# Optimization experiments

Hardware: AMD Instinct MI355X
Metric: run time of the kernel (lower is better)

The kernel has to match this reference:

```python
import jax, jax.numpy as jnp
import numpy as np

H = 32        # num_attention_heads
DN = 128      # qk_nope_head_dim
DR = 64       # qk_rope_head_dim
DV = 128      # v_head_dim
DQ = DN + DR  # q_head_dim
HID = 4096
NEG_INF = -1e30


def setup_inputs() -> dict:
    key = jax.random.key(0)
    k0, k1, k2, k3 = jax.random.split(key, 4)
    B, S = 4, 1024
    hidden_states = jax.random.normal(k0, (B, S, HID), dtype=jnp.float32)
    wq = jax.random.normal(k1, (HID, H * DQ), dtype=jnp.float32) * 0.02
    wkv = jax.random.normal(k2, (HID, H * (DN + DV) + DR), dtype=jnp.float32) * 0.02
    wo = jax.random.normal(k3, (H * DV, HID), dtype=jnp.float32) * 0.02
    return {"hidden_states": hidden_states, "wq": wq, "wkv": wkv, "wo": wo}


def reference(hidden_states, wq, wkv, wo):
    B, S, D = hidden_states.shape
    # q_proj -> [B, S, H, DQ]; attention only uses the nope part q[..., :DN]
    q = jnp.einsum('bsd,de->bse', hidden_states, wq).reshape(B, S, H, DQ)
    kv = jnp.einsum('bsd,de->bse', hidden_states, wkv)
    k = kv[..., : H * DN].reshape(B, S, H, DN)
    v = kv[..., H * DN : H * (DN + DV)].reshape(B, S, H, DV)
    # rope columns kv[..., H*(DN+DV):] are computed by kv_proj but unused, as in source
    scale = DQ ** -0.5  # note: scale uses full q_head_dim (192), per source
    scores = jnp.einsum('bqhd,bkhd->bhqk', q[..., :DN], k) * scale
    causal = jnp.tril(jnp.ones((S, S), dtype=bool))  # [q, k]
    scores = jnp.where(causal[None, None], scores, NEG_INF)
    probs = jax.nn.softmax(scores, axis=-1)
    attn = jnp.einsum('bhqk,bkhd->bqhd', probs, v).reshape(B, S, H * DV)
    return jnp.einsum('bse,ed->bsd', attn, wo)
```

## Files before the change

kernel.cpp:

```cpp
#include <hip/hip_runtime.h>


typedef __attribute__((ext_vector_type(4))) float f32x4;
typedef _Float16 half8 __attribute__((ext_vector_type(8)));
typedef _Float16 half4 __attribute__((ext_vector_type(4)));

#define AS3(p) ((__attribute__((address_space(3))) void*)(p))
#define AS1(p) ((__attribute__((address_space(1))) void*)(void*)(p))

__global__ __launch_bounds__(256) void k_convert(const float* __restrict__ src,
                                                 _Float16* __restrict__ dst) {
  int i = (blockIdx.x * 256 + threadIdx.x) * 8;
  float4 a = *(const float4*)(src + i);
  float4 b = *(const float4*)(src + i + 4);
  half8 v = { (_Float16)a.x, (_Float16)a.y, (_Float16)a.z, (_Float16)a.w,
              (_Float16)b.x, (_Float16)b.y, (_Float16)b.z, (_Float16)b.w };
  *(half8*)(dst + i) = v;
}

__global__ __launch_bounds__(256) void k_tc_qkv(const float* __restrict__ wq,
                                                const float* __restrict__ wkv,
                                                _Float16* __restrict__ out) {
  __shared__ __align__(16) _Float16 t[64][72];
  int k0 = blockIdx.x * 64;
  int c0 = blockIdx.y * 64;
  int tid = threadIdx.x;
  int rl = tid >> 4;
  int cl4 = (tid & 15) << 2;
  int c = c0 + cl4;
#pragma unroll
  for (int i = 0; i < 4; ++i) {
    int r = k0 + rl + i * 16;
    const float* sp;
    if (c0 < 4096) sp = wq + (size_t)r * 6144 + ((c >> 7) * 192 + (c & 127));
    else           sp = wkv + (size_t)r * 8256 + (c - 4096);
    float4 v = *(const float4*)sp;
    t[cl4 + 0][rl + i * 16] = (_Float16)v.x;
    t[cl4 + 1][rl + i * 16] = (_Float16)v.y;
    t[cl4 + 2][rl + i * 16] = (_Float16)v.z;
    t[cl4 + 3][rl + i * 16] = (_Float16)v.w;
  }
  __syncthreads();
  int r4 = (tid & 15) << 2;
#pragma unroll
  for (int i = 0; i < 4; ++i) {
    int cl = (tid >> 4) + i * 16;
    half4 p = { t[cl][r4], t[cl][r4 + 1], t[cl][r4 + 2], t[cl][r4 + 3] };
    *(half4*)(out + (size_t)(c0 + cl) * 4096 + k0 + r4) = p;
  }
}

__global__ __launch_bounds__(256) void k_tc_wo(const float* __restrict__ wo,
                                               _Float16* __restrict__ out) {
  __shared__ __align__(16) _Float16 t[64][72];
  int k0 = blockIdx.x * 64;
  int c0 = blockIdx.y * 64;
  int tid = threadIdx.x;
  int rl = tid >> 4;
  int cl4 = (tid & 15) << 2;
#pragma unroll
  for (int i = 0; i < 4; ++i) {
    int r = k0 + rl + i * 16;
    float4 v = *(const float4*)(wo + (size_t)r * 4096 + c0 + cl4);
    t[cl4 + 0][rl + i * 16] = (_Float16)v.x;
    t[cl4 + 1][rl + i * 16] = (_Float16)v.y;
    t[cl4 + 2][rl + i * 16] = (_Float16)v.z;
    t[cl4 + 3][rl + i * 16] = (_Float16)v.w;
  }
  __syncthreads();
  int r4 = (tid & 15) << 2;
#pragma unroll
  for (int i = 0; i < 4; ++i) {
    int cl = (tid >> 4) + i * 16;
    half4 p = { t[cl][r4], t[cl][r4 + 1], t[cl][r4 + 2], t[cl][r4 + 3] };
    *(half4*)(out + (size_t)(c0 + cl) * 4096 + k0 + r4) = p;
  }
}


#define A_OFF(d, h) ((d) * 32768 + (h) * 16384)
#define B_OFF(d, h) (65536 + (d) * 32768 + (h) * 16384)

#define STAGE(gbase, ldsoff, ktb)                                              \
  do {                                                                         \
    _Pragma("unroll") for (int i_ = 0; i_ < 2; ++i_) {                         \
      int c_ = w * 2 + i_;                                                     \
      int row_ = c_ * 16 + (lane >> 2);                                        \
      int ss_ = (lane & 3) ^ ((lane >> 3) & 3);                                \
      __builtin_amdgcn_global_load_lds(                                        \
          AS1((gbase) + (size_t)row_ * ldb + (ktb) + ss_ * 16),                \
          AS3(lds + (ldsoff) + c_ * 1024), 16, 0, 0);                          \
    }                                                                          \
  } while (0)

#define LDA(dst, d, ks, fm)                                                    \
  do {                                                                         \
    int r_ = wr * 128 + (fm) * 16 + (lane & 15);                               \
    int sl_ = (lane >> 4) ^ ((r_ >> 1) & 3);                                   \
    dst = *(const half8*)(lds + (d) * 32768 + (ks) * 16384 + r_ * 64 +         \
                          sl_ * 16);                                           \
  } while (0)

#define LDB(dst, d, ks, fn)                                                    \
  do {                                                                         \
    int r_ = wc * 64 + (fn) * 16 + (lane & 15);                                \
    int sl_ = (lane >> 4) ^ ((r_ >> 1) & 3);                                   \
    dst = *(const half8*)(lds + 65536 + (d) * 32768 + (ks) * 16384 +           \
                          r_ * 64 + sl_ * 16);                                 \
  } while (0)

#define BARRIER()                                                              \
  do {                                                                         \
    asm volatile("" ::: "memory");                                             \
    __builtin_amdgcn_s_barrier();                                              \
    asm volatile("" ::: "memory");                                             \
  } while (0)

#define MFMA16(mh)                                                             \
  do {                                                                         \
    __builtin_amdgcn_s_setprio(1);                                             \
    _Pragma("unroll") for (int mi_ = 0; mi_ < 4; ++mi_)                        \
        _Pragma("unroll") for (int ni_ = 0; ni_ < 4; ++ni_)                    \
            acc[(mh) * 4 + mi_][ni_] = __builtin_amdgcn_mfma_f32_16x16x32_f16( \
                af[mi_], bfr[ni_], acc[(mh) * 4 + mi_][ni_], 0, 0, 0);         \
    __builtin_amdgcn_s_setprio(0);                                             \
  } while (0)

__global__ __launch_bounds__(512, 2) void k_gemm256(
    const _Float16* __restrict__ A, const _Float16* __restrict__ Bt,
    void* __restrict__ outp, int M, int N, int K, int mode, int ntn, int nblk) {
  extern __shared__ __align__(16) char lds[];
  int tid = threadIdx.x, lane = tid & 63, w = tid >> 6;
  int wr = w >> 2, wc = w & 3;
  int bid = blockIdx.x;
  int sid = (bid & 7) * (nblk >> 3) + (bid >> 3);
  int mt = sid / ntn, nt = sid % ntn;
  int m0 = mt * 256, n0 = nt * 256;

  const char* Ab = (const char*)(A + (size_t)m0 * K);
  const char* Bb = (const char*)(Bt + (size_t)n0 * K);
  size_t ldb = (size_t)K * 2;

  f32x4 acc[8][4];
#pragma unroll
  for (int i = 0; i < 8; ++i)
#pragma unroll
    for (int j = 0; j < 4; ++j) acc[i][j] = (f32x4){0.f, 0.f, 0.f, 0.f};
  half8 af[4], bfr[4];

  int NT = K >> 6;
  STAGE(Ab, A_OFF(0, 0), 0);
  STAGE(Bb, B_OFF(0, 0), 0);
  STAGE(Ab, A_OFF(0, 1), 64);
  STAGE(Bb, B_OFF(0, 1), 64);
  STAGE(Ab, A_OFF(1, 0), 128);
  STAGE(Bb, B_OFF(1, 0), 128);
  asm volatile("s_waitcnt vmcnt(4)" ::: "memory");
  BARRIER();

  for (int k = 0; k < NT; ++k) {
    int d = k & 1, dn = d ^ 1;
    int ktb1 = (k + 1) << 7, ktb2 = (k + 2) << 7;
    bool s1 = (k + 1 < NT), s2 = (k + 2 < NT);
    LDB(bfr[0], d, 0, 0); LDB(bfr[1], d, 0, 1);
    LDB(bfr[2], d, 0, 2); LDB(bfr[3], d, 0, 3);
    LDA(af[0], d, 0, 0); LDA(af[1], d, 0, 1);
    LDA(af[2], d, 0, 2); LDA(af[3], d, 0, 3);
    if (s1) STAGE(Ab, A_OFF(dn, 1), ktb1 + 64);
    BARRIER();
    MFMA16(0);
    BARRIER();
    LDA(af[0], d, 0, 4); LDA(af[1], d, 0, 5);
    LDA(af[2], d, 0, 6); LDA(af[3], d, 0, 7);
    if (s1) STAGE(Bb, B_OFF(dn, 1), ktb1 + 64);
    BARRIER();
    MFMA16(1);
    BARRIER();
    LDB(bfr[0], d, 1, 0); LDB(bfr[1], d, 1, 1);
    LDB(bfr[2], d, 1, 2); LDB(bfr[3], d, 1, 3);
    LDA(af[0], d, 1, 0); LDA(af[1], d, 1, 1);
    LDA(af[2], d, 1, 2); LDA(af[3], d, 1, 3);
    if (s2) STAGE(Ab, A_OFF(d, 0), ktb2);
    BARRIER();
    MFMA16(0);
    BARRIER();
    LDA(af[0], d, 1, 4); LDA(af[1], d, 1, 5);
    LDA(af[2], d, 1, 6); LDA(af[3], d, 1, 7);
    if (s2) {
      STAGE(Bb, B_OFF(d, 0), ktb2);
      asm volatile("s_waitcnt vmcnt(4)" ::: "memory");
    } else {
      asm volatile("s_waitcnt vmcnt(0)" ::: "memory");
    }
    BARRIER();
    MFMA16(1);
    BARRIER();
  }

  if (mode == 2) {
    float* O = (float*)outp;
#pragma unroll
    for (int fm = 0; fm < 8; ++fm)
#pragma unroll
      for (int j = 0; j < 4; ++j) {
        int r = m0 + wr * 128 + fm * 16 + ((lane >> 4) << 2) + j;
        float* op = O + (size_t)r * N + n0 + wc * 64 + (lane & 15);
#pragma unroll
        for (int ni = 0; ni < 4; ++ni) op[ni * 16] = acc[fm][ni][j];
      }
  } else {
    _Float16* Q = (_Float16*)outp;
    _Float16* Kk = Q + 16777216;
    _Float16* Vt = Q + 33554432;
    int cb0 = n0 + wc * 64;
    int seg = cb0 >> 12;
    int h = (cb0 >> 7) & 31;
    int dbase = cb0 & 127;
    if (seg < 2) {
      _Float16* Obuf = (seg == 0) ? Q : Kk;
#pragma unroll
      for (int fm = 0; fm < 8; ++fm) {
        int t0 = m0 + wr * 128 + fm * 16 + ((lane >> 4) << 2);
        int bb = t0 >> 10, s0 = t0 & 1023;
        size_t base = ((size_t)bb * 32 + h) * 1024;
#pragma unroll
        for (int j = 0; j < 4; ++j)
#pragma unroll
          for (int ni = 0; ni < 4; ++ni)
            Obuf[(base + s0 + j) * 128 + dbase + ni * 16 + (lane & 15)] =
                (_Float16)acc[fm][ni][j];
      }
    } else {
#pragma unroll
      for (int fm = 0; fm < 8; ++fm) {
        int t0 = m0 + wr * 128 + fm * 16 + ((lane >> 4) << 2);
        int bb = t0 >> 10, s0 = t0 & 1023;
#pragma unroll
        for (int ni = 0; ni < 4; ++ni) {
          int dd = dbase + ni * 16 + (lane & 15);
          half4 p = { (_Float16)acc[fm][ni][0], (_Float16)acc[fm][ni][1],
                      (_Float16)acc[fm][ni][2], (_Float16)acc[fm][ni][3] };
          *(half4*)(Vt + (((size_t)bb * 32 + h) * 128 + dd) * 1024 + s0) = p;
        }
      }
    }
  }
}

__global__ __launch_bounds__(256) void k_attn(const _Float16* __restrict__ Qb,
                                              const _Float16* __restrict__ Kb,
                                              const _Float16* __restrict__ Vtb,
                                              _Float16* __restrict__ outp) {
  __shared__ __align__(16) _Float16 sK[64][152];
  __shared__ __align__(16) _Float16 sV[128][72];
  __shared__ __align__(16) _Float16 sP[4][16][72];
  const float SCL = 0.10411834905624762f;
  int tid = threadIdx.x;
  int lane = tid & 63;
  int w = tid >> 6;
  int qt = blockIdx.x;
  int h = blockIdx.y;
  int b = blockIdx.z;
  int q0 = qt * 64;
  size_t bh = (size_t)b * 32 + h;
  const _Float16* Qp = Qb + bh * (1024 * 128);
  const _Float16* Kp = Kb + bh * (1024 * 128);
  const _Float16* Vp = Vtb + bh * (128 * 1024);

  half8 aQ[4];
  {
    const _Float16* qr = Qp + (size_t)(q0 + w * 16 + (lane & 15)) * 128 + ((lane >> 4) << 3);
#pragma unroll
    for (int ks = 0; ks < 4; ++ks) aQ[ks] = *(const half8*)(qr + ks * 32);
  }
  f32x4 accO[8];
#pragma unroll
  for (int g = 0; g < 8; ++g) accO[g] = (f32x4){0.f, 0.f, 0.f, 0.f};
  float m_r[4] = { -__builtin_inff(), -__builtin_inff(), -__builtin_inff(), -__builtin_inff() };
  float l_r[4] = { 0.f, 0.f, 0.f, 0.f };

  int ntile = qt + 1;
  int qrb = q0 + w * 16 + ((lane >> 4) << 2);
  for (int kt = 0; kt < ntile; ++kt) {
    int kv0 = kt * 64;
#pragma unroll
    for (int i = 0; i < 4; ++i) {
      int idx = tid + i * 256;
      int r = idx >> 4;
      int cb = (idx & 15) << 3;
      *(int4*)&sK[r][cb] = *(const int4*)(Kp + (size_t)(kv0 + r) * 128 + cb);
    }
#pragma unroll
    for (int i = 0; i < 4; ++i) {
      int idx = tid + i * 256;
      int r = idx >> 3;
      int cb = (idx & 7) << 3;
      *(int4*)&sV[r][cb] = *(const int4*)(Vp + (size_t)r * 1024 + kv0 + cb);
    }
    __syncthreads();
    f32x4 sc[4];
#pragma unroll
    for (int g = 0; g < 4; ++g) {
      f32x4 c = (f32x4){0.f, 0.f, 0.f, 0.f};
#pragma unroll
      for (int ks = 0; ks < 4; ++ks) {
        half8 bk = *(const half8*)&sK[g * 16 + (lane & 15)][ks * 32 + ((lane >> 4) << 3)];
        c = __builtin_amdgcn_mfma_f32_16x16x32_f16(aQ[ks], bk, c, 0, 0, 0);
      }
      sc[g] = c;
    }
    bool diag = (kt == ntile - 1);
    float sv[4][4];
#pragma unroll
    for (int g = 0; g < 4; ++g) {
      int kvc = kv0 + g * 16 + (lane & 15);
#pragma unroll
      for (int j = 0; j < 4; ++j) {
        float s = sc[g][j] * SCL;
        if (diag && kvc > qrb + j) s = -__builtin_inff();
        sv[j][g] = s;
      }
    }
#pragma unroll
    for (int j = 0; j < 4; ++j) {
      float mx = fmaxf(fmaxf(sv[j][0], sv[j][1]), fmaxf(sv[j][2], sv[j][3]));
      mx = fmaxf(mx, __shfl_xor(mx, 1));
      mx = fmaxf(mx, __shfl_xor(mx, 2));
      mx = fmaxf(mx, __shfl_xor(mx, 4));
      mx = fmaxf(mx, __shfl_xor(mx, 8));
      float mnew = fmaxf(m_r[j], mx);
      float corr = exp2f(m_r[j] - mnew);
      m_r[j] = mnew;
      float rs = 0.f;
#pragma unroll
      for (int g = 0; g < 4; ++g) {
        float p = exp2f(sv[j][g] - mnew);
        sv[j][g] = p;
        rs += p;
      }
      rs += __shfl_xor(rs, 1);
      rs += __shfl_xor(rs, 2);
      rs += __shfl_xor(rs, 4);
      rs += __shfl_xor(rs, 8);
      l_r[j] = l_r[j] * corr + rs;
#pragma unroll
      for (int g2 = 0; g2 < 8; ++g2) accO[g2][j] *= corr;
    }
#pragma unroll
    for (int j = 0; j < 4; ++j)
#pragma unroll
      for (int g = 0; g < 4; ++g)
        sP[w][((lane >> 4) << 2) + j][g * 16 + (lane & 15)] = (_Float16)sv[j][g];
    __syncthreads();
#pragma unroll
    for (int ks = 0; ks < 2; ++ks) {
      half8 ap = *(const half8*)&sP[w][lane & 15][ks * 32 + ((lane >> 4) << 3)];
#pragma unroll
      for (int g2 = 0; g2 < 8; ++g2) {
        half8 bv = *(const half8*)&sV[g2 * 16 + (lane & 15)][ks * 32 + ((lane >> 4) << 3)];
        accO[g2] = __builtin_amdgcn_mfma_f32_16x16x32_f16(ap, bv, accO[g2], 0, 0, 0);
      }
    }
    __syncthreads();
  }
  float inv[4];
#pragma unroll
  for (int j = 0; j < 4; ++j) inv[j] = 1.f / l_r[j];
#pragma unroll
  for (int j = 0; j < 4; ++j) {
    size_t rb = ((size_t)b * 1024 + qrb + j) * 4096 + (size_t)h * 128 + (lane & 15);
#pragma unroll
    for (int g2 = 0; g2 < 8; ++g2)
      outp[rb + g2 * 16] = (_Float16)(accO[g2][j] * inv[j]);
  }
}

extern "C" void kernel_launch(void* const* d_in, const int* in_sizes, int n_in,
                              void* d_out, int out_size, void* d_ws, size_t ws_size,
                              hipStream_t stream) {
  const float* hs  = (const float*)d_in[0];
  const float* wq  = (const float*)d_in[1];
  const float* wkv = (const float*)d_in[2];
  const float* wo  = (const float*)d_in[3];
  char* ws = (char*)d_ws;

  const size_t OFF_HS    = 0;
  const size_t OFF_WQKVT = 33554432;
  const size_t OFF_Q     = 134217728;
  const size_t OFF_ATTN  = OFF_WQKVT;
  const size_t OFF_WOT   = OFF_HS;

  _Float16* hs16   = (_Float16*)(ws + OFF_HS);
  _Float16* wqkvT  = (_Float16*)(ws + OFF_WQKVT);
  _Float16* qkv    = (_Float16*)(ws + OFF_Q);
  _Float16* attn   = (_Float16*)(ws + OFF_ATTN);
  _Float16* woT    = (_Float16*)(ws + OFF_WOT);

  hipFuncSetAttribute((const void*)k_gemm256,
                      hipFuncAttributeMaxDynamicSharedMemorySize, 131072);

  k_convert<<<8192, 256, 0, stream>>>(hs, hs16);
  k_tc_qkv<<<dim3(64, 192), 256, 0, stream>>>(wq, wkv, wqkvT);
  k_gemm256<<<768, 512, 131072, stream>>>(hs16, wqkvT, (void*)qkv,
                                          4096, 12288, 4096, 1, 48, 768);
  k_tc_wo<<<dim3(64, 64), 256, 0, stream>>>(wo, woT);
  k_attn<<<dim3(16, 32, 4), 256, 0, stream>>>(qkv, qkv + 16777216, qkv + 33554432, attn);
  k_gemm256<<<256, 512, 131072, stream>>>(attn, woT, d_out,
                                          4096, 4096, 4096, 2, 16, 256);
}
```

Before: 1.088 ms.

## Give each attention wave its own query tile and read K/V from global

The attention kernel no longer has four waves share a 64-row query tile with K and V staged in LDS. Each wave now handles its own 16-row query tile and reads K and V fragments straight from global memory into MFMA operands, which removes the block-wide barriers. Slots are ordered so the longest causal rows are scheduled first, and the grid becomes a flat 1-D launch, to improve load balance. The cost is that K/V reuse across waves in a block is lost, so each wave pulls K/V from L2/HBM itself with less latency hiding.

```diff
diff --git a/kernel.cpp b/kernel.cpp
--- a/kernel.cpp
+++ b/kernel.cpp
@@ -77,7 +77,6 @@
   }
 }
 
-
 #define A_OFF(d, h) ((d) * 32768 + (h) * 16384)
 #define B_OFF(d, h) (65536 + (d) * 32768 + (h) * 16384)
 
@@ -251,25 +250,24 @@
                                               const _Float16* __restrict__ Kb,
                                               const _Float16* __restrict__ Vtb,
                                               _Float16* __restrict__ outp) {
-  __shared__ __align__(16) _Float16 sK[64][152];
-  __shared__ __align__(16) _Float16 sV[128][72];
   __shared__ __align__(16) _Float16 sP[4][16][72];
   const float SCL = 0.10411834905624762f;
   int tid = threadIdx.x;
   int lane = tid & 63;
   int w = tid >> 6;
-  int qt = blockIdx.x;
-  int h = blockIdx.y;
-  int b = blockIdx.z;
-  int q0 = qt * 64;
-  size_t bh = (size_t)b * 32 + h;
-  const _Float16* Qp = Qb + bh * (1024 * 128);
-  const _Float16* Kp = Kb + bh * (1024 * 128);
-  const _Float16* Vp = Vtb + bh * (128 * 1024);
+  int gslot = blockIdx.x * 4 + w;
+  int bh = gslot >> 6;
+  int slot = gslot & 63;
+  int qt = 63 - slot;
+  int q0 = qt * 16;
+  int b = bh >> 5, h = bh & 31;
+  const _Float16* Qp = Qb + (size_t)bh * (1024 * 128);
+  const _Float16* Kp = Kb + (size_t)bh * (1024 * 128);
+  const _Float16* Vp = Vtb + (size_t)bh * (128 * 1024);
 
   half8 aQ[4];
   {
-    const _Float16* qr = Qp + (size_t)(q0 + w * 16 + (lane & 15)) * 128 + ((lane >> 4) << 3);
+    const _Float16* qr = Qp + (size_t)(q0 + (lane & 15)) * 128 + ((lane >> 4) << 3);
 #pragma unroll
     for (int ks = 0; ks < 4; ++ks) aQ[ks] = *(const half8*)(qr + ks * 32);
   }
@@ -279,32 +277,21 @@
   float m_r[4] = { -__builtin_inff(), -__builtin_inff(), -__builtin_inff(), -__builtin_inff() };
   float l_r[4] = { 0.f, 0.f, 0.f, 0.f };
 
-  int ntile = qt + 1;
-  int qrb = q0 + w * 16 + ((lane >> 4) << 2);
+  int ntile = (qt >> 2) + 1;
+  int qrb = q0 + ((lane >> 4) << 2);
+  const _Float16* Kl = Kp + (size_t)(lane & 15) * 128 + ((lane >> 4) << 3);
+  const _Float16* Vl = Vp + (size_t)(lane & 15) * 1024 + ((lane >> 4) << 3);
+
   for (int kt = 0; kt < ntile; ++kt) {
     int kv0 = kt * 64;
-#pragma unroll
-    for (int i = 0; i < 4; ++i) {
-      int idx = tid + i * 256;
-      int r = idx >> 4;
-      int cb = (idx & 15) << 3;
-      *(int4*)&sK[r][cb] = *(const int4*)(Kp + (size_t)(kv0 + r) * 128 + cb);
-    }
-#pragma unroll
-    for (int i = 0; i < 4; ++i) {
-      int idx = tid + i * 256;
-      int r = idx >> 3;
-      int cb = (idx & 7) << 3;
-      *(int4*)&sV[r][cb] = *(const int4*)(Vp + (size_t)r * 1024 + kv0 + cb);
-    }
-    __syncthreads();
     f32x4 sc[4];
 #pragma unroll
     for (int g = 0; g < 4; ++g) {
+      const _Float16* kb = Kl + (size_t)(kv0 + g * 16) * 128;
       f32x4 c = (f32x4){0.f, 0.f, 0.f, 0.f};
 #pragma unroll
       for (int ks = 0; ks < 4; ++ks) {
-        half8 bk = *(const half8*)&sK[g * 16 + (lane & 15)][ks * 32 + ((lane >> 4) << 3)];
+        half8 bk = *(const half8*)(kb + ks * 32);
         c = __builtin_amdgcn_mfma_f32_16x16x32_f16(aQ[ks], bk, c, 0, 0, 0);
       }
       sc[g] = c;
@@ -351,17 +338,15 @@
 #pragma unroll
       for (int g = 0; g < 4; ++g)
         sP[w][((lane >> 4) << 2) + j][g * 16 + (lane & 15)] = (_Float16)sv[j][g];
-    __syncthreads();
 #pragma unroll
     for (int ks = 0; ks < 2; ++ks) {
       half8 ap = *(const half8*)&sP[w][lane & 15][ks * 32 + ((lane >> 4) << 3)];
 #pragma unroll
       for (int g2 = 0; g2 < 8; ++g2) {
-        half8 bv = *(const half8*)&sV[g2 * 16 + (lane & 15)][ks * 32 + ((lane >> 4) << 3)];
+        half8 bv = *(const half8*)(Vl + (size_t)(g2 * 16) * 1024 + kv0 + ks * 32);
         accO[g2] = __builtin_amdgcn_mfma_f32_16x16x32_f16(ap, bv, accO[g2], 0, 0, 0);
       }
     }
-    __syncthreads();
   }
   float inv[4];
 #pragma unroll
@@ -404,7 +389,7 @@
   k_gemm256<<<768, 512, 131072, stream>>>(hs16, wqkvT, (void*)qkv,
                                           4096, 12288, 4096, 1, 48, 768);
   k_tc_wo<<<dim3(64, 64), 256, 0, stream>>>(wo, woT);
-  k_attn<<<dim3(16, 32, 4), 256, 0, stream>>>(qkv, qkv + 16777216, qkv + 33554432, attn);
+  k_attn<<<2048, 256, 0, stream>>>(qkv, qkv + 16777216, qkv + 33554432, attn);
   k_gemm256<<<256, 512, 131072, stream>>>(attn, woT, d_out,
                                           4096, 4096, 4096, 2, 16, 256);
 }
```

Result: slower. 1.366 ms (+25.6%).
